# Optimization experiments

Hardware: AMD Instinct MI355X
Metric: run time of the kernel (lower is better)

Reference implementation:

```python
import jax, jax.numpy as jnp
import numpy as np

EPS = 1e-6


def setup_inputs() -> dict:
    key = jax.random.key(0)
    kx, kp = jax.random.split(key)
    B, D, P = 16384, 1024, 1024
    x = jax.random.normal(kx, (B, D), dtype=jnp.float32)
    prototypes = jax.random.normal(kp, (P, D), dtype=jnp.float32)
    return {"x": x, "prototypes": prototypes}


def reference(x, prototypes):
    # Vectorized form of the per-(sample, prototype) yat similarity:
    #   score[i, j] = <x_i, p_j>^2 / (||x_i - p_j||^2 + eps)
    # x: [B, D], prototypes: [P, D] -> scores: [B, P]
    x_flat = x.reshape(x.shape[0], -1)
    dots = jnp.einsum("bd,pd->bp", x_flat, prototypes)          # [B, P] GEMM
    x_sq = jnp.sum(x_flat * x_flat, axis=-1, keepdims=True)      # [B, 1]
    p_sq = jnp.sum(prototypes * prototypes, axis=-1)[None, :]    # [1, P]
    dist_sq = x_sq + p_sq - 2.0 * dots                            # ||x - p||^2
    scores = (dots * dots) / (dist_sq + EPS)
    return scores.astype(jnp.float32)
```

## Files before the change

kernel.cpp:

```cpp
#include <hip/hip_runtime.h>
#include <hip/hip_bf16.h>

#define EPS 1e-6f

typedef __attribute__((ext_vector_type(8))) __bf16 bf16x8;
typedef __attribute__((ext_vector_type(4))) float f32x4;

__global__ __launch_bounds__(512, 2) void yat_fused(
    const float* __restrict__ X, const float* __restrict__ Pr,
    float* __restrict__ out, int M, int N, int K) {

    __shared__ __align__(128) char sm[131072];
    __shared__ __align__(16) float sqx[256];
    __shared__ __align__(16) float sqp[256];
    const char* smc = (const char*)sm;

    const int t = threadIdx.x;
    const int lane = t & 63;
    const int wid = t >> 6;
    const int wm = wid >> 2;
    const int wn = wid & 3;

    const int nbx = N >> 8;
    const int nby = M >> 8;
    const int total = nbx * nby;
    int bid = blockIdx.x;
    bid = (bid & 7) * (total >> 3) + (bid >> 3);
    const int by = bid / nbx;
    const int bx = bid - by * nbx;
    const int brow = by << 8;
    const int bcol = bx << 8;

    const int NKT = K >> 6;

    f32x4 acc[8][4];
#pragma unroll
    for (int i = 0; i < 8; ++i)
#pragma unroll
        for (int j = 0; j < 4; ++j) acc[i][j] = (f32x4){0.f, 0.f, 0.f, 0.f};

    const int arow = lane & 15;
    const int kq16 = (lane >> 4) * 16;

    const int rsub = lane >> 3;
    const int lcq = (lane & 7) ^ rsub;
    const long baseA = (long)(brow + wid * 8 + rsub) * K + lcq * 8;
    const long baseB = (long)(bcol + wid * 8 + rsub) * K + lcq * 8;
    const long sH = (long)128 * K, sL = (long)64 * K;
    const int dlane = wid * 1024 + lane * 16;

    f32x4 c0[4], c1[4];
    float qA[2][2] = {{0.f, 0.f}, {0.f, 0.f}};
    float qB[2][2] = {{0.f, 0.f}, {0.f, 0.f}};

#define ISSUE(buf, G, BASE, hh, kt) do {                                       \
    const float* g0_ = (G) + BASE + (hh) * sH + (long)(kt) * 64;               \
    buf[0] = *(const f32x4*)(g0_);                                             \
    buf[1] = *(const f32x4*)(g0_ + 4);                                         \
    buf[2] = *(const f32x4*)(g0_ + sL);                                        \
    buf[3] = *(const f32x4*)(g0_ + sL + 4);                                    \
} while (0)

#define WRITE(buf, Q, hh, slot, boff) do {                                     \
    _Pragma("unroll")                                                          \
    for (int l_ = 0; l_ < 2; ++l_) {                                           \
        f32x4 u_ = buf[2 * l_], v_ = buf[2 * l_ + 1];                          \
        Q[hh][l_] += u_[0]*u_[0] + u_[1]*u_[1] + u_[2]*u_[2] + u_[3]*u_[3]     \
                   + v_[0]*v_[0] + v_[1]*v_[1] + v_[2]*v_[2] + v_[3]*v_[3];    \
        bf16x8 pk_;                                                            \
        _Pragma("unroll")                                                      \
        for (int i_ = 0; i_ < 4; ++i_) {                                       \
            pk_[i_]     = (__bf16)u_[i_];                                      \
            pk_[4 + i_] = (__bf16)v_[i_];                                      \
        }                                                                      \
        *(bf16x8*)((char*)sm + (slot) * 65536 + (boff) + (hh) * 16384          \
                   + l_ * 8192 + dlane) = pk_;                                 \
    }                                                                          \
} while (0)

#define READ_A(slot, mh) do {                                                  \
    _Pragma("unroll")                                                          \
    for (int mi_ = 0; mi_ < 4; ++mi_) {                                        \
        int r_ = wm * 128 + (mh) * 64 + mi_ * 16 + arow;                       \
        const char* p_ = smc + (slot) * 65536 + r_ * 128;                      \
        int s_ = (r_ & 7) << 4;                                                \
        af[mi_][0] = *(const bf16x8*)(p_ + (kq16 ^ s_));                       \
        af[mi_][1] = *(const bf16x8*)(p_ + ((64 + kq16) ^ s_));                \
    }                                                                          \
} while (0)

#define READ_B(slot, nh) do {                                                  \
    _Pragma("unroll")                                                          \
    for (int ni_ = 0; ni_ < 2; ++ni_) {                                        \
        int r_ = wn * 64 + (nh) * 32 + ni_ * 16 + arow;                        \
        const char* p_ = smc + (slot) * 65536 + 32768 + r_ * 128;              \
        int s_ = (r_ & 7) << 4;                                                \
        bB[ni_][0] = *(const bf16x8*)(p_ + (kq16 ^ s_));                       \
        bB[ni_][1] = *(const bf16x8*)(p_ + ((64 + kq16) ^ s_));                \
    }                                                                          \
} while (0)

#define MFMA_Q(mh, nh) do {                                                    \
    __builtin_amdgcn_s_setprio(1);                                             \
    _Pragma("unroll")                                                          \
    for (int kk_ = 0; kk_ < 2; ++kk_)                                          \
        _Pragma("unroll")                                                      \
        for (int mi_ = 0; mi_ < 4; ++mi_)                                      \
            _Pragma("unroll")                                                  \
            for (int ni_ = 0; ni_ < 2; ++ni_)                                  \
                acc[(mh) * 4 + mi_][(nh) * 2 + ni_] =                          \
                    __builtin_amdgcn_mfma_f32_16x16x32_bf16(                   \
                        af[mi_][kk_], bB[ni_][kk_],                            \
                        acc[(mh) * 4 + mi_][(nh) * 2 + ni_], 0, 0, 0);         \
    __builtin_amdgcn_s_setprio(0);                                             \
} while (0)

#define PBAR() do {                                                            \
    __builtin_amdgcn_s_barrier();                                              \
    __builtin_amdgcn_sched_barrier(0);                                         \
    asm volatile("" ::: "memory");                                             \
} while (0)
#define LGKMDRAIN() asm volatile("s_waitcnt lgkmcnt(0)" ::: "memory")

    bf16x8 af[4][2];
    bf16x8 bB[2][2];

    ISSUE(c0, X, baseA, 0, 0);
    ISSUE(c1, X, baseA, 1, 0);
    WRITE(c0, qA, 0, 0, 0);
    ISSUE(c0, Pr, baseB, 0, 0);
    WRITE(c1, qA, 1, 0, 0);
    ISSUE(c1, Pr, baseB, 1, 0);
    WRITE(c0, qB, 0, 0, 32768);
    WRITE(c1, qB, 1, 0, 32768);
    if (NKT > 1) ISSUE(c0, X, baseA, 0, 1);
    LGKMDRAIN();
    PBAR();

    for (int kt = 0; kt < NKT; ++kt) {
        const int slot = kt & 1;
        const int nslot = slot ^ 1;
        const bool more = (kt + 1) < NKT;
        const bool more2 = (kt + 2) < NKT;

        if (more) { WRITE(c0, qA, 0, nslot, 0); ISSUE(c1, X, baseA, 1, kt + 1); }
        READ_A(slot, 0); READ_B(slot, 0);
        MFMA_Q(0, 0);
        if (more) { WRITE(c1, qA, 1, nslot, 0); ISSUE(c0, Pr, baseB, 0, kt + 1); }
        READ_B(slot, 1);
        MFMA_Q(0, 1);
        if (more) { WRITE(c0, qB, 0, nslot, 32768); ISSUE(c1, Pr, baseB, 1, kt + 1); }
        READ_A(slot, 1); READ_B(slot, 0);
        MFMA_Q(1, 0);
        if (more) WRITE(c1, qB, 1, nslot, 32768);
        if (more2) ISSUE(c0, X, baseA, 0, kt + 2);
        READ_B(slot, 1);
        MFMA_Q(1, 1);
        LGKMDRAIN();
        PBAR();
    }

#undef ISSUE
#undef WRITE
#undef READ_A
#undef READ_B
#undef MFMA_Q
#undef PBAR
#undef LGKMDRAIN

#pragma unroll
    for (int hh = 0; hh < 2; ++hh)
#pragma unroll
        for (int l = 0; l < 2; ++l) {
            float a = qA[hh][l], b = qB[hh][l];
#pragma unroll
            for (int m = 1; m <= 4; m <<= 1) {
                a += __shfl_xor(a, m);
                b += __shfl_xor(b, m);
            }
            if ((lane & 7) == 0) {
                int r = hh * 128 + l * 64 + wid * 8 + rsub;
                sqx[r] = a;
                sqp[r] = b;
            }
        }

    float* smf = (float*)sm;
#pragma unroll
    for (int pass = 0; pass < 2; ++pass) {
        __syncthreads();
        if (wm == pass) {
#pragma unroll
            for (int ni = 0; ni < 4; ++ni) {
                int lcc = wn * 64 + ni * 16 + arow;
                float ps = sqp[lcc];
#pragma unroll
                for (int mi = 0; mi < 8; ++mi) {
                    f32x4 c = acc[mi][ni];
                    int lr0 = mi * 16 + (lane >> 4) * 4;
                    f32x4 xs4 = *(const f32x4*)(&sqx[pass * 128 + lr0]);
                    int lcs = lcc ^ (((lr0 >> 2) & 1) << 4);
#pragma unroll
                    for (int j = 0; j < 4; ++j) {
                        float dv = c[j];
                        float denom = xs4[j] + ps - 2.0f * dv + EPS;
                        smf[(lr0 + j) * 256 + lcs] = dv * dv / denom;
                    }
                }
            }
        }
        __syncthreads();
#pragma unroll
        for (int rr = 0; rr < 16; ++rr) {
            int r = wid * 16 + rr;
            int swz = ((r >> 2) & 1) << 4;
            int c0l = lane * 4;
            f32x4 v = *(const f32x4*)(smf + r * 256 + (c0l ^ swz));
            *(f32x4*)(out + (size_t)(brow + pass * 128 + r) * N + bcol + c0l) = v;
        }
    }
}

__global__ void yat_fallback(const float* __restrict__ x, const float* __restrict__ p,
                             float* __restrict__ out, int B, int P, int D) {
    __shared__ float xs[1024];
    int b = blockIdx.x;
    int pc = blockIdx.y * 256 + threadIdx.x;
    for (int i = threadIdx.x; i < D; i += 256) xs[i] = x[(size_t)b * D + i];
    __syncthreads();
    if (pc >= P) return;
    float dot = 0.f, psq = 0.f, xsq = 0.f;
    for (int k = 0; k < D; ++k) {
        float pv = p[(size_t)pc * D + k];
        float xv = xs[k];
        dot += xv * pv;
        psq += pv * pv;
        xsq += xv * xv;
    }
    float denom = xsq + psq - 2.f * dot + EPS;
    out[(size_t)b * P + pc] = dot * dot / denom;
}

extern "C" void kernel_launch(void* const* d_in, const int* in_sizes, int n_in,
                              void* d_out, int out_size, void* d_ws, size_t ws_size,
                              hipStream_t stream) {
    const float* x = (const float*)d_in[0];
    const float* p = (const float*)d_in[1];
    float* out = (float*)d_out;

    const int D = 1024;
    const int B = in_sizes[0] / D;
    const int P = in_sizes[1] / D;

    int nblocks = (B / 256) * (P / 256);
    if ((B % 256) || (P % 256) || (D % 64) || (nblocks % 8)) {
        yat_fallback<<<dim3(B, (P + 255) / 256), 256, 0, stream>>>(x, p, out, B, P, D);
        return;
    }

    yat_fused<<<dim3(nblocks), 512, 0, stream>>>(x, p, out, B, P, D);
}
```

Before: 63.61 us.

## Keep both B fragment sets in registers, split global staging finer, add phase barriers

Global-to-LDS staging buffers shrink from four to two f32x4 per buffer. Loads are now issued at half-tile granularity, so each write is followed immediately by the next load. B fragments are held in two register sets, so the second M half reuses them instead of re-reading LDS. Workgroup barriers are inserted between MFMA phases to keep waves in lockstep. The aim is fewer LDS reads and lower register pressure, at the cost of three extra barriers per K iteration.

```diff
diff --git a/kernel.cpp b/kernel.cpp
--- a/kernel.cpp
+++ b/kernel.cpp
@@ -49,33 +49,28 @@
     const long sH = (long)128 * K, sL = (long)64 * K;
     const int dlane = wid * 1024 + lane * 16;
 
-    f32x4 c0[4], c1[4];
+    f32x4 c0[2], c1[2];
     float qA[2][2] = {{0.f, 0.f}, {0.f, 0.f}};
     float qB[2][2] = {{0.f, 0.f}, {0.f, 0.f}};
 
-#define ISSUE(buf, G, BASE, hh, kt) do {                                       \
-    const float* g0_ = (G) + BASE + (hh) * sH + (long)(kt) * 64;               \
+#define ISSUE(buf, G, BASE, hh, l, kt) do {                                    \
+    const float* g0_ = (G) + BASE + (hh) * sH + (l) * sL + (long)(kt) * 64;    \
     buf[0] = *(const f32x4*)(g0_);                                             \
     buf[1] = *(const f32x4*)(g0_ + 4);                                         \
-    buf[2] = *(const f32x4*)(g0_ + sL);                                        \
-    buf[3] = *(const f32x4*)(g0_ + sL + 4);                                    \
-} while (0)
-
-#define WRITE(buf, Q, hh, slot, boff) do {                                     \
-    _Pragma("unroll")                                                          \
-    for (int l_ = 0; l_ < 2; ++l_) {                                           \
-        f32x4 u_ = buf[2 * l_], v_ = buf[2 * l_ + 1];                          \
-        Q[hh][l_] += u_[0]*u_[0] + u_[1]*u_[1] + u_[2]*u_[2] + u_[3]*u_[3]     \
-                   + v_[0]*v_[0] + v_[1]*v_[1] + v_[2]*v_[2] + v_[3]*v_[3];    \
-        bf16x8 pk_;                                                            \
-        _Pragma("unroll")                                                      \
-        for (int i_ = 0; i_ < 4; ++i_) {                                       \
-            pk_[i_]     = (__bf16)u_[i_];                                      \
-            pk_[4 + i_] = (__bf16)v_[i_];                                      \
-        }                                                                      \
-        *(bf16x8*)((char*)sm + (slot) * 65536 + (boff) + (hh) * 16384          \
-                   + l_ * 8192 + dlane) = pk_;                                 \
+} while (0)
+
+#define WRITE(buf, Q, hh, l, slot, boff) do {                                  \
+    f32x4 u_ = buf[0], v_ = buf[1];                                            \
+    Q[hh][l] += u_[0]*u_[0] + u_[1]*u_[1] + u_[2]*u_[2] + u_[3]*u_[3]          \
+              + v_[0]*v_[0] + v_[1]*v_[1] + v_[2]*v_[2] + v_[3]*v_[3];         \
+    bf16x8 pk_;                                                                \
+    _Pragma("unroll")                                                          \
+    for (int i_ = 0; i_ < 4; ++i_) {                                           \
+        pk_[i_]     = (__bf16)u_[i_];                                          \
+        pk_[4 + i_] = (__bf16)v_[i_];                                          \
     }                                                                          \
+    *(bf16x8*)((char*)sm + (slot) * 65536 + (boff) + (hh) * 16384              \
+               + (l) * 8192 + dlane) = pk_;                                    \
 } while (0)
 
 #define READ_A(slot, mh) do {                                                  \
@@ -89,18 +84,18 @@
     }                                                                          \
 } while (0)
 
-#define READ_B(slot, nh) do {                                                  \
+#define READ_B(slot, nh, dst) do {                                             \
     _Pragma("unroll")                                                          \
     for (int ni_ = 0; ni_ < 2; ++ni_) {                                        \
         int r_ = wn * 64 + (nh) * 32 + ni_ * 16 + arow;                        \
         const char* p_ = smc + (slot) * 65536 + 32768 + r_ * 128;              \
         int s_ = (r_ & 7) << 4;                                                \
-        bB[ni_][0] = *(const bf16x8*)(p_ + (kq16 ^ s_));                       \
-        bB[ni_][1] = *(const bf16x8*)(p_ + ((64 + kq16) ^ s_));                \
+        dst[ni_][0] = *(const bf16x8*)(p_ + (kq16 ^ s_));                      \
+        dst[ni_][1] = *(const bf16x8*)(p_ + ((64 + kq16) ^ s_));               \
     }                                                                          \
 } while (0)
 
-#define MFMA_Q(mh, nh) do {                                                    \
+#define MFMA_Q(mh, nh, bset) do {                                              \
     __builtin_amdgcn_s_setprio(1);                                             \
     _Pragma("unroll")                                                          \
     for (int kk_ = 0; kk_ < 2; ++kk_)                                          \
@@ -110,7 +105,7 @@
             for (int ni_ = 0; ni_ < 2; ++ni_)                                  \
                 acc[(mh) * 4 + mi_][(nh) * 2 + ni_] =                          \
                     __builtin_amdgcn_mfma_f32_16x16x32_bf16(                   \
-                        af[mi_][kk_], bB[ni_][kk_],                            \
+                        af[mi_][kk_], bset[ni_][kk_],                          \
                         acc[(mh) * 4 + mi_][(nh) * 2 + ni_], 0, 0, 0);         \
     __builtin_amdgcn_s_setprio(0);                                             \
 } while (0)
@@ -123,17 +118,19 @@
 #define LGKMDRAIN() asm volatile("s_waitcnt lgkmcnt(0)" ::: "memory")
 
     bf16x8 af[4][2];
-    bf16x8 bB[2][2];
-
-    ISSUE(c0, X, baseA, 0, 0);
-    ISSUE(c1, X, baseA, 1, 0);
-    WRITE(c0, qA, 0, 0, 0);
-    ISSUE(c0, Pr, baseB, 0, 0);
-    WRITE(c1, qA, 1, 0, 0);
-    ISSUE(c1, Pr, baseB, 1, 0);
-    WRITE(c0, qB, 0, 0, 32768);
-    WRITE(c1, qB, 1, 0, 32768);
-    if (NKT > 1) ISSUE(c0, X, baseA, 0, 1);
+    bf16x8 bf0[2][2], bf1[2][2];
+
+    ISSUE(c0, X, baseA, 0, 0, 0);
+    ISSUE(c1, X, baseA, 0, 1, 0);
+    WRITE(c0, qA, 0, 0, 0, 0);  ISSUE(c0, X, baseA, 1, 0, 0);
+    WRITE(c1, qA, 0, 1, 0, 0);  ISSUE(c1, X, baseA, 1, 1, 0);
+    WRITE(c0, qA, 1, 0, 0, 0);  ISSUE(c0, Pr, baseB, 0, 0, 0);
+    WRITE(c1, qA, 1, 1, 0, 0);  ISSUE(c1, Pr, baseB, 0, 1, 0);
+    WRITE(c0, qB, 0, 0, 0, 32768);  ISSUE(c0, Pr, baseB, 1, 0, 0);
+    WRITE(c1, qB, 0, 1, 0, 32768);  ISSUE(c1, Pr, baseB, 1, 1, 0);
+    WRITE(c0, qB, 1, 0, 0, 32768);
+    WRITE(c1, qB, 1, 1, 0, 32768);
+    if (NKT > 1) { ISSUE(c0, X, baseA, 0, 0, 1); ISSUE(c1, X, baseA, 0, 1, 1); }
     LGKMDRAIN();
     PBAR();
 
@@ -143,19 +140,30 @@
         const bool more = (kt + 1) < NKT;
         const bool more2 = (kt + 2) < NKT;
 
-        if (more) { WRITE(c0, qA, 0, nslot, 0); ISSUE(c1, X, baseA, 1, kt + 1); }
-        READ_A(slot, 0); READ_B(slot, 0);
-        MFMA_Q(0, 0);
-        if (more) { WRITE(c1, qA, 1, nslot, 0); ISSUE(c0, Pr, baseB, 0, kt + 1); }
-        READ_B(slot, 1);
-        MFMA_Q(0, 1);
-        if (more) { WRITE(c0, qB, 0, nslot, 32768); ISSUE(c1, Pr, baseB, 1, kt + 1); }
-        READ_A(slot, 1); READ_B(slot, 0);
-        MFMA_Q(1, 0);
-        if (more) WRITE(c1, qB, 1, nslot, 32768);
-        if (more2) ISSUE(c0, X, baseA, 0, kt + 2);
-        READ_B(slot, 1);
-        MFMA_Q(1, 1);
+        if (more) {
+            WRITE(c0, qA, 0, 0, nslot, 0);  ISSUE(c0, X, baseA, 1, 0, kt + 1);
+            WRITE(c1, qA, 0, 1, nslot, 0);  ISSUE(c1, X, baseA, 1, 1, kt + 1);
+        }
+        READ_A(slot, 0); READ_B(slot, 0, bf0);
+        MFMA_Q(0, 0, bf0); PBAR();
+        if (more) {
+            WRITE(c0, qA, 1, 0, nslot, 0);  ISSUE(c0, Pr, baseB, 0, 0, kt + 1);
+            WRITE(c1, qA, 1, 1, nslot, 0);  ISSUE(c1, Pr, baseB, 0, 1, kt + 1);
+        }
+        READ_B(slot, 1, bf1);
+        MFMA_Q(0, 1, bf1); PBAR();
+        if (more) {
+            WRITE(c0, qB, 0, 0, nslot, 32768);  ISSUE(c0, Pr, baseB, 1, 0, kt + 1);
+            WRITE(c1, qB, 0, 1, nslot, 32768);  ISSUE(c1, Pr, baseB, 1, 1, kt + 1);
+        }
+        READ_A(slot, 1);
+        MFMA_Q(1, 0, bf0); PBAR();
+        if (more) {
+            WRITE(c0, qB, 1, 0, nslot, 32768);
+            WRITE(c1, qB, 1, 1, nslot, 32768);
+        }
+        if (more2) { ISSUE(c0, X, baseA, 0, 0, kt + 2); ISSUE(c1, X, baseA, 0, 1, kt + 2); }
+        MFMA_Q(1, 1, bf1);
         LGKMDRAIN();
         PBAR();
     }
```

Result: slower. 66.09 us (+3.9%).
